# Performance work log

Measured on AMD Instinct MI355X. Metric: run time of the kernel, lower is better.

## Reference

```python
import jax, jax.numpy as jnp
import numpy as np

# Output volume shape passed as `shape` to forward_3stacks / interpol.grid_push
VOL_SHAPE = (128, 128, 128)


def _grid_push(inp, grid, out_shape):
    """Trilinear scatter-splat (interpol.grid_push, bound=replicate, extrapolate=True).

    inp:  [B, C, D, H, W] values
    grid: [B, D, H, W, 3] target coords in output voxel space, (z, y, x) order
    returns [B, C, *out_shape]
    """
    B, C = inp.shape[0], inp.shape[1]
    S0, S1, S2 = out_shape
    N = inp.shape[2] * inp.shape[3] * inp.shape[4]
    vals = inp.reshape(B, C, N)
    coords = grid.reshape(B, N, 3)

    def push_one(v, g):  # v: [C, N], g: [N, 3]
        g0f = jnp.floor(g)
        f = g - g0f                      # trilinear fractions, [N, 3]
        g0 = g0f.astype(jnp.int32)
        acc = jnp.zeros((C, S0 * S1 * S2), dtype=v.dtype)
        for dz in (0, 1):
            wz = f[:, 0] if dz else 1.0 - f[:, 0]
            iz = jnp.clip(g0[:, 0] + dz, 0, S0 - 1)
            for dy in (0, 1):
                wy = f[:, 1] if dy else 1.0 - f[:, 1]
                iy = jnp.clip(g0[:, 1] + dy, 0, S1 - 1)
                for dx in (0, 1):
                    wx = f[:, 2] if dx else 1.0 - f[:, 2]
                    ix = jnp.clip(g0[:, 2] + dx, 0, S2 - 1)
                    flat = (iz * S1 + iy) * S2 + ix  # [N]
                    w = (wz * wy * wx)[None, :]      # [1, N]
                    acc = acc.at[:, flat].add(v * w)
        return acc.reshape(C, S0, S1, S2)

    return jax.vmap(push_one)(vals, coords)


def setup_inputs() -> dict:
    key = jax.random.key(0)
    k1, k2, k3 = jax.random.split(key, 3)
    x = jax.random.normal(k1, (1, 1, 384, 128, 128), dtype=jnp.float32)
    flow = jax.random.normal(k2, (1, 3, 384, 128, 128), dtype=jnp.float32)
    mask = jax.random.uniform(k3, (1, 1, 384, 128, 128), dtype=jnp.float32)
    return {"x": x, "flow": flow, "mask": mask}


def reference(x, flow, mask):
    """WarpingLayer_3stacks.forward_3stacks with transpose=True, warp=True.

    flow already matches x's spatial shape, so the F.interpolate resize is identity
    (the branch `if flow.shape[2:] != x.shape[2:]` is not taken).
    """
    # per-dim flow rescale: flow[:, d-2] * (x.shape[d]-1)/(flow.shape[d]-1)
    scale = jnp.asarray([(x.shape[d] - 1) / (flow.shape[d] - 1) for d in range(2, 5)],
                        dtype=x.dtype)
    flow = flow * scale[None, :, None, None, None]

    D, H, W = x.shape[2], x.shape[3], x.shape[4]
    gz, gy, gx = jnp.meshgrid(jnp.arange(D, dtype=x.dtype),
                              jnp.arange(H, dtype=x.dtype),
                              jnp.arange(W, dtype=x.dtype), indexing='ij')
    base = jnp.stack([gz, gy, gx], axis=0)          # [3, D, H, W]
    grid = flow + base[None]                        # self.warp * flow + meshgrid
    grid = jnp.transpose(grid, (0, 2, 3, 4, 1))     # [B, D, H, W, 3]

    intensities = jnp.concatenate([x * mask, mask], axis=1)  # [B, 2, D, H, W]
    return _grid_push(intensities, grid, VOL_SHAPE)          # [B, 2, 128, 128, 128]
```

## Files before the change

kernel.cpp:

```cpp
#include <hip/hip_runtime.h>


#define OS    128
#define OS3   (OS * OS * OS)
#define SRC_D 384
#define SRC_H 128
#define SRC_W 128
#define NSRC  (SRC_D * SRC_H * SRC_W)
#define ZSPLIT 128
#define PLANE_CELLS (OS * OS)

#define TZ 4
#define TY 4
#define HALO 3
#define NJOBS 100
#define GITER 7
#define GBLK  1024

#define PGROUPS 128
#define PSPB    2
#define PBLK    (PGROUPS * 4)
#define SLICES  16

#define REG_CAP 512
#define LCAP    65536

#define OFF_CNT    0
#define OFF_COUNTS 1024
#define OFF_REGS   8192
#define OFF_LIST   (OFF_REGS + GBLK * REG_CAP * 16)
#define OFF_TMP    (OFF_LIST + LCAP * 16)
#define OFF_PART   (16 * 1024 * 1024)
#define WS_NEED    (OFF_PART + PGROUPS * 2 * PLANE_CELLS * 4)

#define S_FIX   262144.0f
#define INV_FIX (1.0f / 262144.0f)

__device__ __forceinline__ unsigned long long pack2(float v, float m) {
    int vi = (int)rintf(v * S_FIX);
    int mi = (int)rintf(m * S_FIX);
    return ((unsigned long long)(unsigned)vi << 32) | (unsigned long long)(unsigned)mi;
}

__device__ __forceinline__ int swzq(int c) { return c ^ ((c >> 4) & 7); }

__device__ __forceinline__ void atomAddF(float* p, float v) {
    unsafeAtomicAdd(p, v);
}

__global__ __launch_bounds__(512) void warp_fused(
    const float* __restrict__ x, const float* __restrict__ flow,
    const float* __restrict__ mask, float* __restrict__ out,
    float* __restrict__ partials,
    unsigned* __restrict__ gcnt, int* __restrict__ counts,
    int4* __restrict__ regs, int4* __restrict__ list)
{
    __shared__ unsigned long long sh[4096];
    __shared__ int scnt;

    const int tid = threadIdx.x;
    const int b = blockIdx.x;

    const float4* __restrict__ fz4 = (const float4*)flow;
    const float4* __restrict__ fy4 = (const float4*)(flow + NSRC);
    const float4* __restrict__ fx4 = (const float4*)(flow + 2 * NSRC);
    const float4* __restrict__ m4p = (const float4*)mask;
    const float4* __restrict__ x4p = (const float4*)x;

    if (b < GBLK) {
        if (tid == 0) scnt = 0;
        #pragma unroll
        for (int s = 0; s < (TZ * TY * OS) / 512; ++s)
            sh[tid + s * 512] = 0ull;
        __syncthreads();

        const int z0 = (b & 31) * TZ;
        const int y0 = (b >> 5) * TY;
        const int wq = tid & 31;
        const int slot = tid >> 5;

        for (int it = 0; it < GITER; ++it) {
            int j = it * 16 + slot;
            int dz = j / 10, dyy = j - dz * 10;
            int zzr = z0 - HALO + dz;
            int hhr = y0 - HALO + dyy;
            int zz = min(max(zzr, 0), ZSPLIT - 1);
            int hh = min(max(hhr, 0), OS - 1);
            bool vrow = (j < NJOBS) && (zzr >= 0) && (zzr < ZSPLIT) &&
                        (hhr >= 0) && (hhr < OS);
            bool home = vrow && (zzr >= z0) && (zzr < z0 + TZ) &&
                        (hhr >= y0) && (hhr < y0 + TY);

            int idx4 = (((zz << 14) + (hh << 7)) >> 2) + wq;
            float4 vfz = fz4[idx4];
            float4 vfy = fy4[idx4];
            float4 vfx = fx4[idx4];
            float4 vm  = m4p[idx4];
            float4 vx  = x4p[idx4];

            if (!vrow) continue;

            #pragma unroll
            for (int p = 0; p < 4; ++p) {
                float gz = ((float*)&vfz)[p] + (float)zz;
                float gy = ((float*)&vfy)[p] + (float)hh;
                float fzf = floorf(gz), fyf = floorf(gy);
                float ffz = gz - fzf, ffy = gy - fyf;
                int iz0 = (int)fzf, iy0 = (int)fyf;

                int cz0 = min(max(iz0,     0), OS - 1);
                int cz1 = min(max(iz0 + 1, 0), OS - 1);
                int cy0 = min(max(iy0,     0), OS - 1);
                int cy1 = min(max(iy0 + 1, 0), OS - 1);

                bool zin = (cz1 >= z0) && (cz0 < z0 + TZ);
                bool yin = (cy1 >= y0) && (cy0 < y0 + TY);
                if (!home && !(zin && yin)) continue;

                int w = wq * 4 + p;
                float gx = ((float*)&vfx)[p] + (float)w;
                float fxf = floorf(gx);
                float ffx = gx - fxf;
                int ix0 = (int)fxf;
                int cx0 = min(max(ix0,     0), OS - 1);
                int cx1 = min(max(ix0 + 1, 0), OS - 1);

                float m = ((float*)&vm)[p];
                float v = ((float*)&vx)[p] * m;

                #pragma unroll
                for (int d2 = 0; d2 < 2; ++d2) {
                    int cz = d2 ? cz1 : cz0;
                    float wz = d2 ? ffz : 1.0f - ffz;
                    bool nz = (cz - zz <= HALO) && (zz - cz <= HALO);
                    int uz = cz - z0;
                    #pragma unroll
                    for (int e2 = 0; e2 < 2; ++e2) {
                        int cy = e2 ? cy1 : cy0;
                        float wzy = wz * (e2 ? ffy : 1.0f - ffy);
                        bool ny = (cy - hh <= HALO) && (hh - cy <= HALO);
                        int uy = cy - y0;
                        bool nearc = nz && ny;
                        #pragma unroll
                        for (int f2 = 0; f2 < 2; ++f2) {
                            int cx = f2 ? cx1 : cx0;
                            float wgt = wzy * (f2 ? ffx : 1.0f - ffx);
                            if (nearc) {
                                if ((unsigned)uz < TZ && (unsigned)uy < TY) {
                                    int off = ((uz * TY + uy) << 7) + swzq(cx);
                                    atomicAdd(&sh[off], pack2(v * wgt, m * wgt));
                                }
                            } else if (home) {
                                int4 r;
                                r.x = (cz << 14) + (cy << 7) + cx;
                                r.y = __float_as_int(v * wgt);
                                r.z = __float_as_int(m * wgt);
                                r.w = 0;
                                int s = atomicAdd(&scnt, 1);
                                if (s < REG_CAP) regs[b * REG_CAP + s] = r;
                                else {
                                    unsigned g = atomicAdd(gcnt, 1u);
                                    if (g < LCAP) list[g] = r;
                                }
                            }
                        }
                    }
                }
            }
        }

        __syncthreads();
        if (tid == 0) counts[b] = min(scnt, REG_CAP);

        for (int i = tid; i < TZ * TY * OS; i += 512) {
            int row = i >> 7;
            int c   = i & 127;
            unsigned long long cell = sh[(row << 7) | swzq(c)];
            float v = (float)(int)(cell >> 32) * INV_FIX;
            float m = (float)(int)(unsigned)cell * INV_FIX;
            int uz = row >> 2, uy = row & 3;
            int o = ((z0 + uz) << 14) + ((y0 + uy) << 7) + c;
            out[o]       = v;
            out[OS3 + o] = m;
        }
    } else {
        const int pb = b - GBLK;
        const int g  = pb >> 2;
        const int q  = pb & 3;
        const int ybase = q << 5;
        const int rlo = max(0, ybase - 5);
        const int rhi = min(OS, ybase + 32 + 5);

        #pragma unroll
        for (int s = 0; s < (32 * OS) / 512; ++s)
            sh[tid + s * 512] = 0ull;
        __syncthreads();

        const int wq = tid & 31;
        const int rs = tid >> 5;

        for (int s = 0; s < PSPB; ++s) {
            int z = ZSPLIT + g * PSPB + s;
            for (int rb = 0; rb < 3; ++rb) {
                int r = rlo + rb * 16 + rs;
                bool valid = r < rhi;
                int rc = min(r, OS - 1);
                int idx4 = (((z << 14) + (rc << 7)) >> 2) + wq;
                float4 vfz = fz4[idx4];
                float4 vfy = fy4[idx4];
                float4 vfx = fx4[idx4];
                float4 vm  = m4p[idx4];
                float4 vx  = x4p[idx4];
                if (!valid) continue;
                bool homeRow = ((r >> 5) == q);

                #pragma unroll
                for (int p = 0; p < 4; ++p) {
                    int w = wq * 4 + p;
                    float gz = ((float*)&vfz)[p] + (float)z;
                    float gy = ((float*)&vfy)[p] + (float)r;
                    float gx = ((float*)&vfx)[p] + (float)w;
                    float m  = ((float*)&vm)[p];
                    float v  = ((float*)&vx)[p] * m;

                    float fyf = floorf(gy), fxf = floorf(gx);
                    float ffy = gy - fyf, ffx = gx - fxf;
                    int iy0 = (int)fyf, ix0 = (int)fxf;
                    int cy0 = min(max(iy0,     0), OS - 1);
                    int cy1 = min(max(iy0 + 1, 0), OS - 1);
                    int cx0 = min(max(ix0,     0), OS - 1);
                    int cx1 = min(max(ix0 + 1, 0), OS - 1);
                    int sx0 = swzq(cx0), sx1 = swzq(cx1);

                    if (gz >= (float)(OS - 1)) {
                        float wy0 = 1.0f - ffy, wy1 = ffy;
                        float wx0 = 1.0f - ffx, wx1 = ffx;

                        int u0 = cy0 - ybase;
                        bool n0 = (cy0 - r <= 5) && (r - cy0 <= 5);
                        if (n0 && (unsigned)u0 < 32u) {
                            unsigned long long* row = &sh[u0 << 7];
                            atomicAdd(&row[sx0], pack2(v * wy0 * wx0, m * wy0 * wx0));
                            atomicAdd(&row[sx1], pack2(v * wy0 * wx1, m * wy0 * wx1));
                        }
                        int u1 = cy1 - ybase;
                        bool n1 = (cy1 - r <= 5) && (r - cy1 <= 5);
                        if (n1 && (unsigned)u1 < 32u) {
                            unsigned long long* row = &sh[u1 << 7];
                            atomicAdd(&row[sx0], pack2(v * wy1 * wx0, m * wy1 * wx0));
                            atomicAdd(&row[sx1], pack2(v * wy1 * wx1, m * wy1 * wx1));
                        }
                        if (homeRow && (!n0 || !n1)) {
                            const int pbase = (OS - 1) << 14;
                            #pragma unroll
                            for (int e2 = 0; e2 < 2; ++e2) {
                                bool far = e2 ? !n1 : !n0;
                                if (!far) continue;
                                int cy = e2 ? cy1 : cy0;
                                float wy = e2 ? wy1 : wy0;
                                unsigned base = atomicAdd(gcnt, 2u);
                                #pragma unroll
                                for (int f2 = 0; f2 < 2; ++f2) {
                                    unsigned slt = base + f2;
                                    if (slt < LCAP) {
                                        float wgt = wy * (f2 ? wx1 : wx0);
                                        int4 qq;
                                        qq.x = pbase + (cy << 7) + (f2 ? cx1 : cx0);
                                        qq.y = __float_as_int(v * wgt);
                                        qq.z = __float_as_int(m * wgt);
                                        qq.w = 0;
                                        list[slt] = qq;
                                    }
                                }
                            }
                        }
                    } else if (homeRow) {
                        float fzf = floorf(gz);
                        float ffz = gz - fzf;
                        int iz0 = (int)fzf;
                        unsigned base = atomicAdd(gcnt, 8u);
                        int t = 0;
                        #pragma unroll
                        for (int d2 = 0; d2 < 2; ++d2) {
                            int cz = min(max(iz0 + d2, 0), OS - 1);
                            float wz = d2 ? ffz : 1.0f - ffz;
                            #pragma unroll
                            for (int e2 = 0; e2 < 2; ++e2) {
                                int cy = e2 ? cy1 : cy0;
                                float wzy = wz * (e2 ? ffy : 1.0f - ffy);
                                #pragma unroll
                                for (int f2 = 0; f2 < 2; ++f2) {
                                    int cx = f2 ? cx1 : cx0;
                                    float wgt = wzy * (f2 ? ffx : 1.0f - ffx);
                                    unsigned slt = base + t;
                                    if (slt < LCAP) {
                                        int4 qq;
                                        qq.x = (cz << 14) + (cy << 7) + cx;
                                        qq.y = __float_as_int(v * wgt);
                                        qq.z = __float_as_int(m * wgt);
                                        qq.w = 0;
                                        list[slt] = qq;
                                    }
                                    ++t;
                                }
                            }
                        }
                    }
                }
            }
        }

        __syncthreads();

        float* dst0 = partials + (size_t)g * 2 * PLANE_CELLS;
        float* dst1 = dst0 + PLANE_CELLS;
        for (int i = tid; i < 32 * OS; i += 512) {
            int row = i >> 7, c = i & 127;
            unsigned long long cell = sh[(row << 7) | swzq(c)];
            float v = (float)(int)(cell >> 32) * INV_FIX;
            float m = (float)(int)(unsigned)cell * INV_FIX;
            int o = ((ybase + row) << 7) + c;
            dst0[o] = v;
            dst1[o] = m;
        }
    }
}

__global__ __launch_bounds__(256) void plane_reduce1(
    const float4* __restrict__ partials, float4* __restrict__ tmp)
{
    int t = blockIdx.x * 256 + threadIdx.x;
    int slice = t >> 13;
    int rem = t & 8191;
    int ch = rem >> 12;
    int c4 = rem & 4095;
    float4 s = make_float4(0, 0, 0, 0);
    #pragma unroll
    for (int g = 0; g < PGROUPS / SLICES; ++g) {
        float4 v = partials[((size_t)((slice * (PGROUPS / SLICES) + g) * 2 + ch)) * 4096 + c4];
        s.x += v.x; s.y += v.y; s.z += v.z; s.w += v.w;
    }
    tmp[(size_t)(slice * 2 + ch) * 4096 + c4] = s;
}

__global__ __launch_bounds__(256) void finalize(
    float* __restrict__ out, const float4* __restrict__ tmp,
    const unsigned* __restrict__ gcnt, const int* __restrict__ counts,
    const int4* __restrict__ regs, const int4* __restrict__ list)
{
    int b = blockIdx.x;
    if (b < 32) {
        int t = b * 256 + threadIdx.x;
        int ch = t >> 12;
        int c4 = t & 4095;
        float4 s = make_float4(0, 0, 0, 0);
        #pragma unroll
        for (int sl = 0; sl < SLICES; ++sl) {
            float4 v = tmp[(size_t)(sl * 2 + ch) * 4096 + c4];
            s.x += v.x; s.y += v.y; s.z += v.z; s.w += v.w;
        }
        float* base = out + ch * OS3 + ((OS - 1) << 14) + c4 * 4;
        atomAddF(base + 0, s.x);
        atomAddF(base + 1, s.y);
        atomAddF(base + 2, s.z);
        atomAddF(base + 3, s.w);
    } else if (b < 32 + GBLK) {
        int rb = b - 32;
        int n = counts[rb];
        const int4* r = regs + (size_t)rb * REG_CAP;
        for (int i = threadIdx.x; i < n; i += 256) {
            int4 q = r[i];
            atomAddF(out + q.x,       __int_as_float(q.y));
            atomAddF(out + OS3 + q.x, __int_as_float(q.z));
        }
    } else {
        unsigned n = *gcnt;
        if (n > LCAP) n = LCAP;
        for (unsigned i = (unsigned)(b - 32 - GBLK) * 256 + threadIdx.x;
             i < n; i += 8 * 256) {
            int4 q = list[i];
            atomAddF(out + q.x,       __int_as_float(q.y));
            atomAddF(out + OS3 + q.x, __int_as_float(q.z));
        }
    }
}

__global__ __launch_bounds__(256) void warp_push_naive(
    const float* __restrict__ x, const float* __restrict__ flow,
    const float* __restrict__ mask, float* __restrict__ out, int N)
{
    int idx = blockIdx.x * blockDim.x + threadIdx.x;
    if (idx >= N) return;
    int w = idx & 127, h = (idx >> 7) & 127, z = idx >> 14;
    float gz = flow[idx] + (float)z;
    float gy = flow[N + idx] + (float)h;
    float gx = flow[2 * N + idx] + (float)w;
    float m = mask[idx];
    float v0 = x[idx] * m;
    float fz0 = floorf(gz), fy0 = floorf(gy), fx0 = floorf(gx);
    float fz = gz - fz0, fy = gy - fy0, fx = gx - fx0;
    int iz0 = (int)fz0, iy0 = (int)fy0, ix0 = (int)fx0;
    #pragma unroll
    for (int dz = 0; dz < 2; ++dz) {
        int cz = min(max(iz0 + dz, 0), OS - 1);
        float wz = dz ? fz : 1.0f - fz;
        #pragma unroll
        for (int dy = 0; dy < 2; ++dy) {
            int cy = min(max(iy0 + dy, 0), OS - 1);
            float wzy = wz * (dy ? fy : 1.0f - fy);
            #pragma unroll
            for (int dx = 0; dx < 2; ++dx) {
                int cx = min(max(ix0 + dx, 0), OS - 1);
                float wgt = wzy * (dx ? fx : 1.0f - fx);
                int o = (cz << 14) + (cy << 7) + cx;
                atomAddF(out + o,       v0 * wgt);
                atomAddF(out + OS3 + o, m * wgt);
            }
        }
    }
}

extern "C" void kernel_launch(void* const* d_in, const int* in_sizes, int n_in,
                              void* d_out, int out_size, void* d_ws, size_t ws_size,
                              hipStream_t stream) {
    (void)in_sizes; (void)n_in; (void)out_size;
    const float* x    = (const float*)d_in[0];
    const float* flow = (const float*)d_in[1];
    const float* mask = (const float*)d_in[2];
    float* out = (float*)d_out;

    if (ws_size >= (size_t)WS_NEED) {
        char* wsb = (char*)d_ws;
        unsigned* gcnt = (unsigned*)(wsb + OFF_CNT);
        int* counts    = (int*)(wsb + OFF_COUNTS);
        int4* regs     = (int4*)(wsb + OFF_REGS);
        int4* list     = (int4*)(wsb + OFF_LIST);
        float4* tmp    = (float4*)(wsb + OFF_TMP);
        float* parts   = (float*)(wsb + OFF_PART);

        hipMemsetAsync(d_ws, 0, 64, stream);

        warp_fused<<<GBLK + PBLK, 512, 0, stream>>>(
            x, flow, mask, out, parts, gcnt, counts, regs, list);
        plane_reduce1<<<512, 256, 0, stream>>>((const float4*)parts, tmp);
        finalize<<<32 + GBLK + 8, 256, 0, stream>>>(
            out, (const float4*)tmp, gcnt, counts, regs, list);
    } else {
        hipMemsetAsync(d_out, 0, (size_t)2 * OS3 * sizeof(float), stream);
        warp_push_naive<<<NSRC / 256, 256, 0, stream>>>(x, flow, mask, out, NSRC);
    }
}
```

Measured before the change: 205.5 us.

## Enlarge gather tiles, fold plane reduction into finalize, trim fixed-point packing

Doubles the z extent of each gather tile (TZ 4 to 8), halving the gather block count and lowering the fraction of redundant halo rows each block must read. The separate plane_reduce1 launch is removed, and finalize now sums all 128 partial planes per cell directly. Fixed-point packing scales v and m once per source voxel and truncates with a cast instead of rintf. Costs: more halo jobs per block, fewer blocks to fill the GPU, and rounding now truncates toward zero, which changes the numerics slightly.

```diff
diff --git a/kernel.cpp b/kernel.cpp
--- a/kernel.cpp
+++ b/kernel.cpp
@@ -10,35 +10,33 @@
 #define ZSPLIT 128
 #define PLANE_CELLS (OS * OS)
 
-#define TZ 4
+#define TZ 8
 #define TY 4
 #define HALO 3
-#define NJOBS 100
-#define GITER 7
-#define GBLK  1024
+#define NJOBS 140
+#define GITER 9
+#define GBLK  512
 
 #define PGROUPS 128
 #define PSPB    2
 #define PBLK    (PGROUPS * 4)
-#define SLICES  16
-
-#define REG_CAP 512
+
+#define REG_CAP 1024
 #define LCAP    65536
 
 #define OFF_CNT    0
 #define OFF_COUNTS 1024
 #define OFF_REGS   8192
 #define OFF_LIST   (OFF_REGS + GBLK * REG_CAP * 16)
-#define OFF_TMP    (OFF_LIST + LCAP * 16)
 #define OFF_PART   (16 * 1024 * 1024)
 #define WS_NEED    (OFF_PART + PGROUPS * 2 * PLANE_CELLS * 4)
 
 #define S_FIX   262144.0f
 #define INV_FIX (1.0f / 262144.0f)
 
-__device__ __forceinline__ unsigned long long pack2(float v, float m) {
-    int vi = (int)rintf(v * S_FIX);
-    int mi = (int)rintf(m * S_FIX);
+__device__ __forceinline__ unsigned long long packt(float a, float b) {
+    int vi = (int)a;
+    int mi = (int)b;
     return ((unsigned long long)(unsigned)vi << 32) | (unsigned long long)(unsigned)mi;
 }
 
@@ -70,12 +68,12 @@
     if (b < GBLK) {
         if (tid == 0) scnt = 0;
         #pragma unroll
-        for (int s = 0; s < (TZ * TY * OS) / 512; ++s)
+        for (int s = 0; s < 4096 / 512; ++s)
             sh[tid + s * 512] = 0ull;
         __syncthreads();
 
-        const int z0 = (b & 31) * TZ;
-        const int y0 = (b >> 5) * TY;
+        const int z0 = (b & 15) * TZ;
+        const int y0 = (b >> 4) * TY;
         const int wq = tid & 31;
         const int slot = tid >> 5;
 
@@ -127,6 +125,8 @@
 
                 float m = ((float*)&vm)[p];
                 float v = ((float*)&vx)[p] * m;
+                float v_s = v * S_FIX;
+                float m_s = m * S_FIX;
 
                 #pragma unroll
                 for (int d2 = 0; d2 < 2; ++d2) {
@@ -148,7 +148,7 @@
                             if (nearc) {
                                 if ((unsigned)uz < TZ && (unsigned)uy < TY) {
                                     int off = ((uz * TY + uy) << 7) + swzq(cx);
-                                    atomicAdd(&sh[off], pack2(v * wgt, m * wgt));
+                                    atomicAdd(&sh[off], packt(v_s * wgt, m_s * wgt));
                                 }
                             } else if (home) {
                                 int4 r;
@@ -192,7 +192,7 @@
         const int rhi = min(OS, ybase + 32 + 5);
 
         #pragma unroll
-        for (int s = 0; s < (32 * OS) / 512; ++s)
+        for (int s = 0; s < 4096 / 512; ++s)
             sh[tid + s * 512] = 0ull;
         __syncthreads();
 
@@ -235,20 +235,24 @@
                     if (gz >= (float)(OS - 1)) {
                         float wy0 = 1.0f - ffy, wy1 = ffy;
                         float wx0 = 1.0f - ffx, wx1 = ffx;
+                        float v_s = v * S_FIX;
+                        float m_s = m * S_FIX;
 
                         int u0 = cy0 - ybase;
                         bool n0 = (cy0 - r <= 5) && (r - cy0 <= 5);
                         if (n0 && (unsigned)u0 < 32u) {
                             unsigned long long* row = &sh[u0 << 7];
-                            atomicAdd(&row[sx0], pack2(v * wy0 * wx0, m * wy0 * wx0));
-                            atomicAdd(&row[sx1], pack2(v * wy0 * wx1, m * wy0 * wx1));
+                            float a = v_s * wy0, bb = m_s * wy0;
+                            atomicAdd(&row[sx0], packt(a * wx0, bb * wx0));
+                            atomicAdd(&row[sx1], packt(a * wx1, bb * wx1));
                         }
                         int u1 = cy1 - ybase;
                         bool n1 = (cy1 - r <= 5) && (r - cy1 <= 5);
                         if (n1 && (unsigned)u1 < 32u) {
                             unsigned long long* row = &sh[u1 << 7];
-                            atomicAdd(&row[sx0], pack2(v * wy1 * wx0, m * wy1 * wx0));
-                            atomicAdd(&row[sx1], pack2(v * wy1 * wx1, m * wy1 * wx1));
+                            float a = v_s * wy1, bb = m_s * wy1;
+                            atomicAdd(&row[sx0], packt(a * wx0, bb * wx0));
+                            atomicAdd(&row[sx1], packt(a * wx1, bb * wx1));
                         }
                         if (homeRow && (!n0 || !n1)) {
                             const int pbase = (OS - 1) << 14;
@@ -326,46 +330,25 @@
     }
 }
 
-__global__ __launch_bounds__(256) void plane_reduce1(
-    const float4* __restrict__ partials, float4* __restrict__ tmp)
-{
-    int t = blockIdx.x * 256 + threadIdx.x;
-    int slice = t >> 13;
-    int rem = t & 8191;
-    int ch = rem >> 12;
-    int c4 = rem & 4095;
-    float4 s = make_float4(0, 0, 0, 0);
-    #pragma unroll
-    for (int g = 0; g < PGROUPS / SLICES; ++g) {
-        float4 v = partials[((size_t)((slice * (PGROUPS / SLICES) + g) * 2 + ch)) * 4096 + c4];
-        s.x += v.x; s.y += v.y; s.z += v.z; s.w += v.w;
-    }
-    tmp[(size_t)(slice * 2 + ch) * 4096 + c4] = s;
-}
-
+#define RBLK 128
 __global__ __launch_bounds__(256) void finalize(
-    float* __restrict__ out, const float4* __restrict__ tmp,
+    float* __restrict__ out, const float* __restrict__ partials,
     const unsigned* __restrict__ gcnt, const int* __restrict__ counts,
     const int4* __restrict__ regs, const int4* __restrict__ list)
 {
     int b = blockIdx.x;
-    if (b < 32) {
+    if (b < RBLK) {
         int t = b * 256 + threadIdx.x;
-        int ch = t >> 12;
-        int c4 = t & 4095;
-        float4 s = make_float4(0, 0, 0, 0);
-        #pragma unroll
-        for (int sl = 0; sl < SLICES; ++sl) {
-            float4 v = tmp[(size_t)(sl * 2 + ch) * 4096 + c4];
-            s.x += v.x; s.y += v.y; s.z += v.z; s.w += v.w;
-        }
-        float* base = out + ch * OS3 + ((OS - 1) << 14) + c4 * 4;
-        atomAddF(base + 0, s.x);
-        atomAddF(base + 1, s.y);
-        atomAddF(base + 2, s.z);
-        atomAddF(base + 3, s.w);
-    } else if (b < 32 + GBLK) {
-        int rb = b - 32;
+        int ch   = t >> 14;
+        int cell = t & 16383;
+        const float* p = partials + (size_t)ch * PLANE_CELLS + cell;
+        float s = 0.0f;
+        #pragma unroll 8
+        for (int g = 0; g < PGROUPS; ++g)
+            s += p[(size_t)g * 2 * PLANE_CELLS];
+        atomAddF(out + ch * OS3 + ((OS - 1) << 14) + cell, s);
+    } else if (b < RBLK + GBLK) {
+        int rb = b - RBLK;
         int n = counts[rb];
         const int4* r = regs + (size_t)rb * REG_CAP;
         for (int i = threadIdx.x; i < n; i += 256) {
@@ -376,7 +359,7 @@
     } else {
         unsigned n = *gcnt;
         if (n > LCAP) n = LCAP;
-        for (unsigned i = (unsigned)(b - 32 - GBLK) * 256 + threadIdx.x;
+        for (unsigned i = (unsigned)(b - RBLK - GBLK) * 256 + threadIdx.x;
              i < n; i += 8 * 256) {
             int4 q = list[i];
             atomAddF(out + q.x,       __int_as_float(q.y));
@@ -435,16 +418,14 @@
         int* counts    = (int*)(wsb + OFF_COUNTS);
         int4* regs     = (int4*)(wsb + OFF_REGS);
         int4* list     = (int4*)(wsb + OFF_LIST);
-        float4* tmp    = (float4*)(wsb + OFF_TMP);
         float* parts   = (float*)(wsb + OFF_PART);
 
         hipMemsetAsync(d_ws, 0, 64, stream);
 
         warp_fused<<<GBLK + PBLK, 512, 0, stream>>>(
             x, flow, mask, out, parts, gcnt, counts, regs, list);
-        plane_reduce1<<<512, 256, 0, stream>>>((const float4*)parts, tmp);
-        finalize<<<32 + GBLK + 8, 256, 0, stream>>>(
-            out, (const float4*)tmp, gcnt, counts, regs, list);
+        finalize<<<RBLK + GBLK + 8, 256, 0, stream>>>(
+            out, parts, gcnt, counts, regs, list);
     } else {
         hipMemsetAsync(d_out, 0, (size_t)2 * OS3 * sizeof(float), stream);
         warp_push_naive<<<NSRC / 256, 256, 0, stream>>>(x, flow, mask, out, NSRC);
```

After: 192.8 us. 6.2% less time.
